# Optimization experiments

Measured on AMD Instinct MI355X. Metric: run time of the kernel, lower is better.

## Reference

```python
import jax, jax.numpy as jnp
import numpy as np

V, D, NH, T_MAX, L, MLP = 50257, 1024, 16, 1024, 12, 4
HD = D // NH
F = D * MLP
B, T = 2, 1024


def setup_inputs() -> dict:
    key = jax.random.key(0)
    ks = jax.random.split(key, 16)
    s = 0.02
    inp = {
        'tokens': jax.random.randint(ks[0], (B, T), 0, V, dtype=jnp.int32),
        'wte': jax.random.normal(ks[1], (V, D), jnp.float32) * s,
        'wpe': jax.random.normal(ks[2], (T_MAX, D), jnp.float32) * s,
        'ln1_w': jnp.ones((L, D)), 'ln1_b': jnp.zeros((L, D)),
        'attn_w': jax.random.normal(ks[3], (L, D, 3 * D), jnp.float32) * s,
        'attn_b': jnp.zeros((L, 3 * D)),
        'aproj_w': jax.random.normal(ks[4], (L, D, D), jnp.float32) * s,
        'aproj_b': jnp.zeros((L, D)),
        'ln2_w': jnp.ones((L, D)), 'ln2_b': jnp.zeros((L, D)),
        'fc_w': jax.random.normal(ks[5], (L, D, F), jnp.float32) * s,
        'fc_b': jnp.zeros((L, F)),
        'proj_w': jax.random.normal(ks[6], (L, F, D), jnp.float32) * s,
        'proj_b': jnp.zeros((L, D)),
        'lnf_w': jnp.ones((D,)), 'lnf_b': jnp.zeros((D,)),
    }
    return inp


def _ln(x, w, b, eps=1e-5):
    m = jnp.mean(x, -1, keepdims=True)
    v = jnp.var(x, -1, keepdims=True)
    return (x - m) * jax.lax.rsqrt(v + eps) * w + b


def _forward(tokens, wte, wpe, ln1_w, ln1_b, attn_w, attn_b, aproj_w, aproj_b,
             ln2_w, ln2_b, fc_w, fc_b, proj_w, proj_b, lnf_w, lnf_b):
    b, t = tokens.shape
    x = wte[tokens] + wpe[:t]  # [B,T,D]
    scale = HD ** -0.5
    causal = jnp.tril(jnp.ones((t, t), bool))  # [T,T]

    def block(x, p):
        l1w, l1b, aw, ab, apw, apb, l2w, l2b, fw, fb, pw, pb = p
        h = _ln(x, l1w, l1b)
        qkv = h @ aw + ab  # [B,T,3D]
        q, k, v = jnp.split(qkv, 3, axis=-1)
        # rearrange 'b t (h n) -> b n t h' with n=NH: last dim is (head_size, n_heads)
        def split_heads(u):
            return u.reshape(b, t, HD, NH).transpose(0, 3, 1, 2)  # [B,NH,T,HD]
        q, k, v = split_heads(q), split_heads(k), split_heads(v)
        scores = jnp.einsum('bnth,bnsh->bnts', q, k) * scale
        scores = jnp.where(causal, scores, -jnp.inf)
        w = jax.nn.softmax(scores, axis=-1)
        att = jnp.einsum('bnts,bnsh->bnth', w, v)
        # rearrange 'b n t h -> b t (n h)'
        att = att.transpose(0, 2, 1, 3).reshape(b, t, D)
        x = x + (att @ apw + apb)
        h2 = _ln(x, l2w, l2b)
        x = x + (jax.nn.gelu(h2 @ fw + fb, approximate=False) @ pw + pb)
        return x, None

    params = (ln1_w, ln1_b, attn_w, attn_b, aproj_w, aproj_b,
              ln2_w, ln2_b, fc_w, fc_b, proj_w, proj_b)
    x, _ = jax.lax.scan(block, x, params)
    x = _ln(x, lnf_w, lnf_b)[:, -1:, :]  # [B,1,D]
    return x @ wte.T  # tied lm_head -> [B,1,V]


def reference(tokens, wte, wpe, ln1_w, ln1_b, attn_w, attn_b, aproj_w, aproj_b,
              ln2_w, ln2_b, fc_w, fc_b, proj_w, proj_b, lnf_w, lnf_b):
    return _forward(tokens, wte, wpe, ln1_w, ln1_b, attn_w, attn_b, aproj_w,
                    aproj_b, ln2_w, ln2_b, fc_w, fc_b, proj_w, proj_b, lnf_w, lnf_b)
```

## Files before the change

kernel.cpp:

```cpp
#include <hip/hip_runtime.h>
#include <cstdint>
#include <math.h>


using u16 = unsigned short;
using bf16x8 = __attribute__((ext_vector_type(8))) short;
using f32x4 = __attribute__((ext_vector_type(4))) float;

#define GLDS16(g, l)                                                        \
  __builtin_amdgcn_global_load_lds(                                         \
      (const __attribute__((address_space(1))) void*)(g),                   \
      (__attribute__((address_space(3))) void*)(l), 16, 0, 0)

__device__ __forceinline__ u16 f2bf(float f) {
  union { float f; unsigned u; } t; t.f = f;
  unsigned r = t.u + 0x7fffu + ((t.u >> 16) & 1u);
  return (u16)(r >> 16);
}
__device__ __forceinline__ float bf2f(u16 v) {
  union { unsigned u; float f; } t; t.u = ((unsigned)v) << 16;
  return t.f;
}

__device__ __forceinline__ float fast_erf(float x) {
  float ax = fabsf(x);
  float t = 1.f / (1.f + 0.3275911f * ax);
  float y = t * (0.254829592f +
            t * (-0.284496736f +
            t * (1.421413741f +
            t * (-1.453152027f +
            t * 1.061405429f))));
  float r = 1.f - y * __expf(-ax * ax);
  return copysignf(r, x);
}

#define DD 1024
#define TTT 1024
#define MR 2048
#define FFF 4096
#define VVV 50257

__global__ __launch_bounds__(256) void k_embed(const int* __restrict__ tokens,
                                               const float* __restrict__ wte,
                                               const float* __restrict__ wpe,
                                               float* __restrict__ x) {
  int m = blockIdx.x, d = threadIdx.x * 4;
  int t = m & (TTT - 1);
  int tok = tokens[m];
  const float4 a = *(const float4*)(wte + (size_t)tok * DD + d);
  const float4 p = *(const float4*)(wpe + (size_t)t * DD + d);
  float4 o; o.x = a.x + p.x; o.y = a.y + p.y; o.z = a.z + p.z; o.w = a.w + p.w;
  *(float4*)(x + (size_t)m * DD + d) = o;
}

__device__ __forceinline__ void addln_body(float* __restrict__ x,
                                           const u16* __restrict__ pp, int npart,
                                           const float* __restrict__ w,
                                           const float* __restrict__ b,
                                           u16* __restrict__ out, int blk) {
  const int wid = threadIdx.x >> 6, lane = threadIdx.x & 63;
  const int m = blk * 4 + wid;
  float* row = x + (size_t)m * DD;
  float4 v[4];
  float s = 0.f, q = 0.f;
#pragma unroll
  for (int j = 0; j < 4; ++j) {
    v[j] = *(const float4*)(row + j * 256 + lane * 4);
#pragma unroll 4
    for (int p = 0; p < npart; ++p) {
      uint64_t pv = *(const uint64_t*)(pp + (size_t)p * MR * DD + (size_t)m * DD + j * 256 + lane * 4);
      v[j].x += bf2f((u16)(pv));
      v[j].y += bf2f((u16)(pv >> 16));
      v[j].z += bf2f((u16)(pv >> 32));
      v[j].w += bf2f((u16)(pv >> 48));
    }
    if (npart) *(float4*)(row + j * 256 + lane * 4) = v[j];
    s += v[j].x + v[j].y + v[j].z + v[j].w;
    q += v[j].x * v[j].x + v[j].y * v[j].y + v[j].z * v[j].z + v[j].w * v[j].w;
  }
#pragma unroll
  for (int off = 1; off < 64; off <<= 1) { s += __shfl_xor(s, off); q += __shfl_xor(q, off); }
  float mean = s * (1.f / DD);
  float var = q * (1.f / DD) - mean * mean;
  float rs = rsqrtf(var + 1e-5f);
#pragma unroll
  for (int j = 0; j < 4; ++j) {
    const float4 wv = *(const float4*)(w + j * 256 + lane * 4);
    const float4 bv = *(const float4*)(b + j * 256 + lane * 4);
    u16 o[4];
    o[0] = f2bf((v[j].x - mean) * rs * wv.x + bv.x);
    o[1] = f2bf((v[j].y - mean) * rs * wv.y + bv.y);
    o[2] = f2bf((v[j].z - mean) * rs * wv.z + bv.z);
    o[3] = f2bf((v[j].w - mean) * rs * wv.w + bv.w);
    *(uint64_t*)(out + (size_t)m * DD + j * 256 + lane * 4) = *(uint64_t*)o;
  }
}

__global__ __launch_bounds__(256) void k_addln(float* __restrict__ x,
                                               const u16* __restrict__ pp, int npart,
                                               const float* __restrict__ w,
                                               const float* __restrict__ b,
                                               u16* __restrict__ out) {
  addln_body(x, pp, npart, w, b, out, blockIdx.x);
}

__device__ __forceinline__ void wtrans_body(const float* __restrict__ atw,
                                            const float* __restrict__ apw,
                                            const float* __restrict__ fcw,
                                            const float* __restrict__ pjw,
                                            u16* __restrict__ wt, int id) {
  __shared__ u16 tb[64][72];
  const float* W; u16* Wt; int K, N, local, kts; bool perm = false;
  if (id < 768)       { W = atw; Wt = wt;           K = 1024; N = 3072; local = id;        kts = 4; perm = true; }
  else if (id < 1024) { W = apw; Wt = wt + 3145728; K = 1024; N = 1024; local = id - 768;  kts = 4; }
  else if (id < 2048) { W = fcw; Wt = wt + 4194304; K = 1024; N = 4096; local = id - 1024; kts = 4; }
  else                { W = pjw; Wt = wt + 8388608; K = 4096; N = 1024; local = id - 2048; kts = 6; }
  const int k0 = (local & ((1 << kts) - 1)) * 64, n0 = (local >> kts) * 64;
  const int tid = threadIdx.x;
  const int rr = tid >> 4, c4 = (tid & 15) * 4;
#pragma unroll
  for (int i = 0; i < 4; ++i) {
    const int r = rr + i * 16;
    const float4 v = *(const float4*)(W + (size_t)(k0 + r) * N + n0 + c4);
    tb[c4 + 0][r] = f2bf(v.x);
    tb[c4 + 1][r] = f2bf(v.y);
    tb[c4 + 2][r] = f2bf(v.z);
    tb[c4 + 3][r] = f2bf(v.w);
  }
  __syncthreads();
  const int n = tid >> 3, k8 = (tid & 7) * 8;
#pragma unroll
  for (int s = 0; s < 2; ++s) {
    u16 o[8];
#pragma unroll
    for (int j = 0; j < 8; ++j) o[j] = tb[n + s * 32][k8 + j];
    int orow = n0 + n + s * 32;
    if (perm) {
      int part = orow >> 10, w = orow & 1023;
      orow = part * 1024 + (w & 15) * 64 + (w >> 4);
    }
    *(bf16x8*)(Wt + (size_t)orow * K + k0 + k8) = *(bf16x8*)o;
  }
}

__global__ __launch_bounds__(256) void k_prep(float* __restrict__ x,
                                              const u16* __restrict__ pp, int npart,
                                              const float* __restrict__ w,
                                              const float* __restrict__ b,
                                              u16* __restrict__ out,
                                              const float* __restrict__ atw,
                                              const float* __restrict__ apw,
                                              const float* __restrict__ fcw,
                                              const float* __restrict__ pjw,
                                              u16* __restrict__ wt,
                                              const float* __restrict__ ab,
                                              float* __restrict__ pbias) {
  if (blockIdx.x < 512) {
    addln_body(x, pp, npart, w, b, out, blockIdx.x);
  } else if (blockIdx.x == 3584) {
    for (int c = threadIdx.x; c < 3072; c += 256) {
      int part = c >> 10, ww = c & 1023;
      pbias[c] = ab[part * 1024 + (ww & 63) * 16 + (ww >> 6)];
    }
  } else {
    wtrans_body(atw, apw, fcw, pjw, wt, blockIdx.x - 512);
  }
}

template <int EPI>
__global__ __launch_bounds__(256) void k_gemm(const u16* __restrict__ A,
                                              const u16* __restrict__ Bt,
                                              const float* __restrict__ bias,
                                              u16* __restrict__ outb,
                                              u16* __restrict__ pp,
                                              u16* __restrict__ vt,
                                              int M, int N, int K, int KC) {
  __shared__ u16 smem[4][128 * 64];
  const int nbx = gridDim.x, nby = gridDim.y;
  const int nwg = nbx * nby * gridDim.z;
  const int orig = blockIdx.x + nbx * (blockIdx.y + nby * blockIdx.z);
  const int qq = nwg >> 3, rr = nwg & 7;
  const int xcd = orig & 7, pos = orig >> 3;
  const int wg = (xcd < rr ? xcd * (qq + 1) : rr * (qq + 1) + (xcd - rr) * qq) + pos;
  const int bx = wg % nbx;
  const int tmpw = wg / nbx;
  const int by = tmpw % nby, bz = tmpw / nby;

  const int tid = threadIdx.x;
  const int lane = tid & 63, wid = tid >> 6;
  const int wr = wid >> 1, wc = wid & 1;
  const int l15 = lane & 15, l4 = lane >> 4;
  const int sx = l15 & 7;
  const int m0 = bx * 128, n0 = by * 128;
  f32x4 acc[4][4] = {};

  const int srow = tid >> 3;
  const int scol = (((tid & 7) ^ (srow & 7)) * 8);
  const int k0beg = bz * KC;
  const int nt = KC >> 6;

  const u16* Ap = A + (size_t)(m0 + srow) * K + scol;
  const u16* Bp = Bt + (size_t)(n0 + srow) * K + scol;

#define STAGE(buf, k0)                                                      \
  {                                                                         \
    _Pragma("unroll")                                                       \
    for (int it = 0; it < 4; ++it) {                                        \
      GLDS16(Ap + (size_t)it * 32 * K + (k0), (char*)smem[buf] + it * 4096 + tid * 16); \
      GLDS16(Bp + (size_t)it * 32 * K + (k0), (char*)smem[2 + (buf)] + it * 4096 + tid * 16); \
    }                                                                       \
  }

  STAGE(0, k0beg);
  for (int t = 0; t < nt; ++t) {
    if (t + 1 < nt) {
      STAGE((t + 1) & 1, k0beg + (t + 1) * 64);
      asm volatile("s_waitcnt vmcnt(8)" ::: "memory");
    } else {
      asm volatile("s_waitcnt vmcnt(0)" ::: "memory");
    }
    __builtin_amdgcn_sched_barrier(0);
    __builtin_amdgcn_s_barrier();
    __builtin_amdgcn_sched_barrier(0);
    const u16* Ab = smem[t & 1];
    const u16* Bb = smem[2 + (t & 1)];
#pragma unroll
    for (int ks = 0; ks < 2; ++ks) {
      const int ch = ((ks * 4 + l4) ^ sx) * 8;
      bf16x8 af[4], bfr[4];
#pragma unroll
      for (int i = 0; i < 4; ++i)
        af[i] = *(const bf16x8*)(Ab + (wr * 64 + i * 16 + l15) * 64 + ch);
#pragma unroll
      for (int j = 0; j < 4; ++j)
        bfr[j] = *(const bf16x8*)(Bb + (wc * 64 + j * 16 + l15) * 64 + ch);
      __builtin_amdgcn_s_setprio(1);
#pragma unroll
      for (int i = 0; i < 4; ++i)
#pragma unroll
        for (int j = 0; j < 4; ++j)
          acc[i][j] = __builtin_amdgcn_mfma_f32_16x16x32_bf16(af[i], bfr[j], acc[i][j], 0, 0, 0);
      __builtin_amdgcn_s_setprio(0);
    }
    __builtin_amdgcn_sched_barrier(0);
    __builtin_amdgcn_s_barrier();
    __builtin_amdgcn_sched_barrier(0);
  }
#undef STAGE
  u16* eb = (u16*)smem;
#pragma unroll
  for (int j = 0; j < 4; ++j) {
    const int col = wc * 64 + j * 16 + l15;
    const float bs = (EPI == 4 && bz != 0) ? 0.f : bias[n0 + col];
#pragma unroll
    for (int i = 0; i < 4; ++i) {
#pragma unroll
      for (int r = 0; r < 4; ++r) {
        const int row = wr * 64 + i * 16 + l4 * 4 + r;
        float v = acc[i][j][r] + bs;
        if (EPI == 2) v = 0.5f * v * (1.f + fast_erf(v * 0.70710678118f));
        eb[row * 132 + col] = f2bf(v);
      }
    }
  }
  __syncthreads();
  if (EPI == 0 && by >= 16) {
    const int b = m0 >> 10, t0 = m0 & 1023;
    const int col = tid >> 1;
    const int tseg = tid & 1;
    const int gc = n0 + col - 2048;
    const int n = gc >> 6, hh = gc & 63;
    u16* vdst = vt + (((size_t)(b * 16 + n)) * 64 + hh) * TTT + t0 + tseg * 64;
    const u16* es = eb + (tseg * 64) * 132 + col;
#pragma unroll
    for (int s = 0; s < 8; ++s) {
      u16 o[8];
#pragma unroll
      for (int k = 0; k < 8; ++k) o[k] = es[(s * 8 + k) * 132];
      *(bf16x8*)(vdst + s * 8) = *(bf16x8*)o;
    }
  } else {
    const int erow = tid >> 1;
    const int ecol0 = (tid & 1) * 64;
    u16* gout = (EPI == 4) ? (pp + (size_t)bz * M * N) : outb;
    u16* gdst = gout + (size_t)(m0 + erow) * N + n0 + ecol0;
    const u16* esrc = eb + erow * 132 + ecol0;
#pragma unroll
    for (int c = 0; c < 8; ++c)
      *(bf16x8*)(gdst + c * 8) = *(const bf16x8*)(esrc + c * 8);
  }
}

__global__ __launch_bounds__(256) void k_attn(const u16* __restrict__ qkv,
                                              const u16* __restrict__ Vt,
                                              u16* __restrict__ attout) {
  __shared__ u16 Ks[128 * 64];
  __shared__ u16 Vs[64 * 128];
  __shared__ u16 Ps[4][16 * 136];

  const int tid = threadIdx.x;
  const int lane = tid & 63, wid = tid >> 6;
  const int l15 = lane & 15, l4 = lane >> 4;
  const int bn = blockIdx.x;
  const int qtr = 15 - (int)blockIdx.y;
  const int q0 = qtr * 64;
  const int b = bn >> 4, nh = bn & 15;
  const char* Kg0 = (const char*)(qkv + (size_t)b * TTT * 3072 + 1024 + nh * 64);
  const char* Vg0 = (const char*)(Vt + (size_t)bn * 64 * TTT);
  const float CEXP = 0.125f * 1.44269504f;

  int KL[4], Kro[4], Kcb[4], VL[4], Voff[4];
#pragma unroll
  for (int it = 0; it < 4; ++it) {
    int L = it * 4096 + tid * 16;
    KL[it] = L;
    int Ls = L ^ (((L >> 7) & 7) << 4);
    Kro[it] = Ls >> 7; Kcb[it] = Ls & 127;
    VL[it] = L;
    int Ls2 = L ^ (((L >> 8) & 7) << 4);
    Voff[it] = (Ls2 >> 8) * 2048 + (Ls2 & 255);
  }

  const int qrow = q0 + wid * 16 + l15;
  const u16* qsrc = qkv + (size_t)(b * TTT + qrow) * 3072 + nh * 64;
  bf16x8 aq[2];
#pragma unroll
  for (int ks = 0; ks < 2; ++ks)
    aq[ks] = *(const bf16x8*)(qsrc + ks * 32 + l4 * 8);

  float m_run[4], l_part[4];
  f32x4 o[4] = {};
#pragma unroll
  for (int r = 0; r < 4; ++r) { m_run[r] = -1e30f; l_part[r] = 0.f; }

  const int ntk = (qtr >> 1) + 1;
  bf16x8 kreg[4], vreg[4];
#pragma unroll
  for (int it = 0; it < 4; ++it) {
    kreg[it] = *(const bf16x8*)(Kg0 + (size_t)Kro[it] * 6144 + Kcb[it]);
    vreg[it] = *(const bf16x8*)(Vg0 + Voff[it]);
  }
  for (int kt = 0; kt < ntk; ++kt) {
#pragma unroll
    for (int it = 0; it < 4; ++it) {
      *(bf16x8*)((char*)Ks + KL[it]) = kreg[it];
      *(bf16x8*)((char*)Vs + VL[it]) = vreg[it];
    }
    __syncthreads();
    if (kt + 1 < ntk) {
#pragma unroll
      for (int it = 0; it < 4; ++it) {
        kreg[it] = *(const bf16x8*)(Kg0 + (size_t)((kt + 1) * 128 + Kro[it]) * 6144 + Kcb[it]);
        vreg[it] = *(const bf16x8*)(Vg0 + (kt + 1) * 256 + Voff[it]);
      }
    }

    f32x4 sf[8];
#pragma unroll
    for (int cf = 0; cf < 8; ++cf) {
      f32x4 z = {};
#pragma unroll
      for (int ks = 0; ks < 2; ++ks) {
        int P = (cf * 16 + l15) * 128 + (ks * 32 + l4 * 8) * 2;
        bf16x8 kb = *(const bf16x8*)((const char*)Ks + (P ^ (((P >> 7) & 7) << 4)));
        z = __builtin_amdgcn_mfma_f32_16x16x32_bf16(aq[ks], kb, z, 0, 0, 0);
      }
      sf[cf] = z;
    }
    if (kt == ntk - 1) {
#pragma unroll
      for (int cf = 0; cf < 8; ++cf)
#pragma unroll
        for (int r = 0; r < 4; ++r) {
          int kg = kt * 128 + cf * 16 + l15;
          int qg = q0 + wid * 16 + l4 * 4 + r;
          if (kg > qg) sf[cf][r] = -1e30f;
        }
    }
    float fac[4];
#pragma unroll
    for (int r = 0; r < 4; ++r) {
      float tm = fmaxf(fmaxf(fmaxf(sf[0][r], sf[1][r]), fmaxf(sf[2][r], sf[3][r])),
                       fmaxf(fmaxf(sf[4][r], sf[5][r]), fmaxf(sf[6][r], sf[7][r])));
#pragma unroll
      for (int off = 1; off < 16; off <<= 1) tm = fmaxf(tm, __shfl_xor(tm, off));
      if (tm > m_run[r] + 64.f) {
        fac[r] = exp2f((m_run[r] - tm) * CEXP);
        m_run[r] = tm;
      } else {
        fac[r] = 1.f;
      }
      float ps = 0.f;
#pragma unroll
      for (int cf = 0; cf < 8; ++cf) {
        float p = exp2f((sf[cf][r] - m_run[r]) * CEXP);
        sf[cf][r] = p;
        ps += p;
      }
      l_part[r] = l_part[r] * fac[r] + ps;
    }
#pragma unroll
    for (int cf = 0; cf < 8; ++cf)
#pragma unroll
      for (int r = 0; r < 4; ++r)
        Ps[wid][(l4 * 4 + r) * 136 + cf * 16 + l15] = f2bf(sf[cf][r]);
#pragma unroll
    for (int hf = 0; hf < 4; ++hf)
#pragma unroll
      for (int r = 0; r < 4; ++r) o[hf][r] *= fac[r];
    bf16x8 pa[4];
#pragma unroll
    for (int ks = 0; ks < 4; ++ks)
      pa[ks] = *(const bf16x8*)&Ps[wid][l15 * 136 + ks * 32 + l4 * 8];
#pragma unroll
    for (int hf = 0; hf < 4; ++hf) {
#pragma unroll
      for (int ks = 0; ks < 4; ++ks) {
        int P = (hf * 16 + l15) * 256 + (ks * 32 + l4 * 8) * 2;
        bf16x8 vb = *(const bf16x8*)((const char*)Vs + (P ^ (((P >> 8) & 7) << 4)));
        o[hf] = __builtin_amdgcn_mfma_f32_16x16x32_bf16(pa[ks], vb, o[hf], 0, 0, 0);
      }
    }
    __syncthreads();
  }
  float lsum[4];
#pragma unroll
  for (int r = 0; r < 4; ++r) {
    float s = l_part[r];
#pragma unroll
    for (int off = 1; off < 16; off <<= 1) s += __shfl_xor(s, off);
    lsum[r] = s;
  }
#pragma unroll
  for (int hf = 0; hf < 4; ++hf)
#pragma unroll
    for (int r = 0; r < 4; ++r) {
      float val = o[hf][r] / lsum[r];
      size_t row = (size_t)b * TTT + q0 + wid * 16 + l4 * 4 + r;
      attout[row * DD + nh * 64 + hf * 16 + l15] = f2bf(val);
    }
}

__global__ __launch_bounds__(256) void k_head(const float* __restrict__ x,
                                              const u16* __restrict__ pp, int npart,
                                              const float* __restrict__ lnf_w,
                                              const float* __restrict__ lnf_b,
                                              const float* __restrict__ wte,
                                              float* __restrict__ out) {
  __shared__ float xs[2 * DD];
  __shared__ float sm[8];
  int tid = threadIdx.x;
  int wid = tid >> 6, lane = tid & 63;
#pragma unroll
  for (int bb = 0; bb < 2; ++bb) {
    int m = bb * TTT + (TTT - 1);
    float4 v = *(const float4*)(x + (size_t)m * DD + tid * 4);
#pragma unroll 4
    for (int p = 0; p < npart; ++p) {
      uint64_t pv = *(const uint64_t*)(pp + (size_t)p * MR * DD + (size_t)m * DD + tid * 4);
      v.x += bf2f((u16)(pv));
      v.y += bf2f((u16)(pv >> 16));
      v.z += bf2f((u16)(pv >> 32));
      v.w += bf2f((u16)(pv >> 48));
    }
    float s = v.x + v.y + v.z + v.w;
    float q = v.x * v.x + v.y * v.y + v.z * v.z + v.w * v.w;
#pragma unroll
    for (int off = 1; off < 64; off <<= 1) { s += __shfl_xor(s, off); q += __shfl_xor(q, off); }
    if ((tid & 63) == 0) { sm[wid] = s; sm[4 + wid] = q; }
    __syncthreads();
    s = sm[0] + sm[1] + sm[2] + sm[3];
    q = sm[4] + sm[5] + sm[6] + sm[7];
    float mean = s * (1.f / DD);
    float var = q * (1.f / DD) - mean * mean;
    float rs = rsqrtf(var + 1e-5f);
    const float4 wv = *(const float4*)(lnf_w + tid * 4);
    const float4 bv = *(const float4*)(lnf_b + tid * 4);
    float4 o;
    o.x = (v.x - mean) * rs * wv.x + bv.x;
    o.y = (v.y - mean) * rs * wv.y + bv.y;
    o.z = (v.z - mean) * rs * wv.z + bv.z;
    o.w = (v.w - mean) * rs * wv.w + bv.w;
    *(float4*)(xs + bb * DD + tid * 4) = o;
    __syncthreads();
  }
  for (int v = blockIdx.x * 4 + wid; v < VVV; v += gridDim.x * 4) {
    const float* wr = wte + (size_t)v * DD;
    float a0 = 0.f, a1 = 0.f;
#pragma unroll
    for (int j = 0; j < 4; ++j) {
      const float4 wv = *(const float4*)(wr + lane * 16 + j * 4);
      const float4 x0 = *(const float4*)(xs + lane * 16 + j * 4);
      const float4 x1 = *(const float4*)(xs + DD + lane * 16 + j * 4);
      a0 += wv.x * x0.x + wv.y * x0.y + wv.z * x0.z + wv.w * x0.w;
      a1 += wv.x * x1.x + wv.y * x1.y + wv.z * x1.z + wv.w * x1.w;
    }
#pragma unroll
    for (int off = 1; off < 64; off <<= 1) { a0 += __shfl_xor(a0, off); a1 += __shfl_xor(a1, off); }
    if (lane == 0) { out[v] = a0; out[VVV + v] = a1; }
  }
}

extern "C" void kernel_launch(void* const* d_in, const int* in_sizes, int n_in,
                              void* d_out, int out_size, void* d_ws, size_t ws_size,
                              hipStream_t stream) {
  const int* tokens    = (const int*)d_in[0];
  const float* wte     = (const float*)d_in[1];
  const float* wpe     = (const float*)d_in[2];
  const float* ln1_w   = (const float*)d_in[3];
  const float* ln1_b   = (const float*)d_in[4];
  const float* attn_w  = (const float*)d_in[5];
  const float* attn_b  = (const float*)d_in[6];
  const float* aproj_w = (const float*)d_in[7];
  const float* aproj_b = (const float*)d_in[8];
  const float* ln2_w   = (const float*)d_in[9];
  const float* ln2_b   = (const float*)d_in[10];
  const float* fc_w    = (const float*)d_in[11];
  const float* fc_b    = (const float*)d_in[12];
  const float* proj_w  = (const float*)d_in[13];
  const float* proj_b  = (const float*)d_in[14];
  const float* lnf_w   = (const float*)d_in[15];
  const float* lnf_b   = (const float*)d_in[16];

  char* ws = (char*)d_ws;
  float* x    = (float*)(ws);
  u16* h      = (u16*)(ws + (8u << 20));
  u16* wt     = (u16*)(ws + (12u << 20));
  u16* qkv    = (u16*)(ws + (36u << 20));
  u16* Vt     = (u16*)(ws + (52u << 20));
  u16* attb   = (u16*)(ws + (56u << 20));
  u16* mlph   = (u16*)(ws + (36u << 20));
  u16* pp     = (u16*)(ws + (60u << 20));
  float* pbias = (float*)(ws + (92u << 20));
  float* out  = (float*)d_out;

  u16* atw = wt;
  u16* apw = wt + 3145728;
  u16* fcw = wt + 4194304;
  u16* pjw = wt + 8388608;

  k_embed<<<MR, 256, 0, stream>>>(tokens, wte, wpe, x);

  for (int l = 0; l < 12; ++l) {
    k_prep<<<3585, 256, 0, stream>>>(x, pp, l == 0 ? 0 : 4,
                                     ln1_w + l * DD, ln1_b + l * DD, h,
                                     attn_w + (size_t)l * DD * 3 * DD,
                                     aproj_w + (size_t)l * DD * DD,
                                     fc_w + (size_t)l * DD * FFF,
                                     proj_w + (size_t)l * FFF * DD, wt,
                                     attn_b + (size_t)l * 3 * DD, pbias);
    k_gemm<0><<<dim3(16, 24, 1), 256, 0, stream>>>(h, atw, pbias, qkv, nullptr, Vt, MR, 3072, 1024, 1024);
    k_attn<<<dim3(32, 16), 256, 0, stream>>>(qkv, Vt, attb);
    k_gemm<4><<<dim3(16, 8, 4), 256, 0, stream>>>(attb, apw, aproj_b + (size_t)l * DD, nullptr, pp, nullptr, MR, 1024, 1024, 256);
    k_addln<<<512, 256, 0, stream>>>(x, pp, 4, ln2_w + l * DD, ln2_b + l * DD, h);
    k_gemm<2><<<dim3(16, 32, 1), 256, 0, stream>>>(h, fcw, fc_b + (size_t)l * FFF, mlph, nullptr, nullptr, MR, 4096, 1024, 1024);
    k_gemm<4><<<dim3(16, 8, 4), 256, 0, stream>>>(mlph, pjw, proj_b + (size_t)l * DD, nullptr, pp, nullptr, MR, 1024, 4096, 1024);
  }
  k_head<<<512, 256, 0, stream>>>(x, pp, 4, lnf_w, lnf_b, wte, out);
}
```

Before: 1.759 ms.

## Fuse embedding into first prep kernel and halve split-K partitions

The standalone embedding kernel is removed; the first layer's prep kernel now computes wte+wpe directly inside the LayerNorm body, which saves one launch and one read of x. The split-K factor for the attention-projection and MLP-projection GEMMs drops from 4 to 2. This halves the bf16 partial buffers written by those GEMMs and read by the add+LayerNorm and head kernels. The cost is fewer blocks in the projection GEMMs (256 instead of 512), which may lower occupancy on the many-CU device.

Result: no change. 1.732 ms (-1.5%).

```diff
diff --git a/kernel.cpp b/kernel.cpp
--- a/kernel.cpp
+++ b/kernel.cpp
@@ -40,43 +40,48 @@
 #define FFF 4096
 #define VVV 50257
 
-__global__ __launch_bounds__(256) void k_embed(const int* __restrict__ tokens,
-                                               const float* __restrict__ wte,
-                                               const float* __restrict__ wpe,
-                                               float* __restrict__ x) {
-  int m = blockIdx.x, d = threadIdx.x * 4;
-  int t = m & (TTT - 1);
-  int tok = tokens[m];
-  const float4 a = *(const float4*)(wte + (size_t)tok * DD + d);
-  const float4 p = *(const float4*)(wpe + (size_t)t * DD + d);
-  float4 o; o.x = a.x + p.x; o.y = a.y + p.y; o.z = a.z + p.z; o.w = a.w + p.w;
-  *(float4*)(x + (size_t)m * DD + d) = o;
-}
-
 __device__ __forceinline__ void addln_body(float* __restrict__ x,
                                            const u16* __restrict__ pp, int npart,
                                            const float* __restrict__ w,
                                            const float* __restrict__ b,
-                                           u16* __restrict__ out, int blk) {
+                                           u16* __restrict__ out, int blk,
+                                           const int* __restrict__ tokens,
+                                           const float* __restrict__ wte,
+                                           const float* __restrict__ wpe,
+                                           int emb) {
   const int wid = threadIdx.x >> 6, lane = threadIdx.x & 63;
   const int m = blk * 4 + wid;
   float* row = x + (size_t)m * DD;
   float4 v[4];
   float s = 0.f, q = 0.f;
-#pragma unroll
-  for (int j = 0; j < 4; ++j) {
-    v[j] = *(const float4*)(row + j * 256 + lane * 4);
-#pragma unroll 4
-    for (int p = 0; p < npart; ++p) {
-      uint64_t pv = *(const uint64_t*)(pp + (size_t)p * MR * DD + (size_t)m * DD + j * 256 + lane * 4);
-      v[j].x += bf2f((u16)(pv));
-      v[j].y += bf2f((u16)(pv >> 16));
-      v[j].z += bf2f((u16)(pv >> 32));
-      v[j].w += bf2f((u16)(pv >> 48));
-    }
-    if (npart) *(float4*)(row + j * 256 + lane * 4) = v[j];
-    s += v[j].x + v[j].y + v[j].z + v[j].w;
-    q += v[j].x * v[j].x + v[j].y * v[j].y + v[j].z * v[j].z + v[j].w * v[j].w;
+  if (emb) {
+    const int tok = tokens[m];
+    const int t = m & (TTT - 1);
+#pragma unroll
+    for (int j = 0; j < 4; ++j) {
+      const float4 a = *(const float4*)(wte + (size_t)tok * DD + j * 256 + lane * 4);
+      const float4 p = *(const float4*)(wpe + (size_t)t * DD + j * 256 + lane * 4);
+      v[j].x = a.x + p.x; v[j].y = a.y + p.y; v[j].z = a.z + p.z; v[j].w = a.w + p.w;
+      *(float4*)(row + j * 256 + lane * 4) = v[j];
+      s += v[j].x + v[j].y + v[j].z + v[j].w;
+      q += v[j].x * v[j].x + v[j].y * v[j].y + v[j].z * v[j].z + v[j].w * v[j].w;
+    }
+  } else {
+#pragma unroll
+    for (int j = 0; j < 4; ++j) {
+      v[j] = *(const float4*)(row + j * 256 + lane * 4);
+#pragma unroll 2
+      for (int p = 0; p < npart; ++p) {
+        uint64_t pv = *(const uint64_t*)(pp + (size_t)p * MR * DD + (size_t)m * DD + j * 256 + lane * 4);
+        v[j].x += bf2f((u16)(pv));
+        v[j].y += bf2f((u16)(pv >> 16));
+        v[j].z += bf2f((u16)(pv >> 32));
+        v[j].w += bf2f((u16)(pv >> 48));
+      }
+      if (npart) *(float4*)(row + j * 256 + lane * 4) = v[j];
+      s += v[j].x + v[j].y + v[j].z + v[j].w;
+      q += v[j].x * v[j].x + v[j].y * v[j].y + v[j].z * v[j].z + v[j].w * v[j].w;
+    }
   }
 #pragma unroll
   for (int off = 1; off < 64; off <<= 1) { s += __shfl_xor(s, off); q += __shfl_xor(q, off); }
@@ -101,7 +106,7 @@
                                                const float* __restrict__ w,
                                                const float* __restrict__ b,
                                                u16* __restrict__ out) {
-  addln_body(x, pp, npart, w, b, out, blockIdx.x);
+  addln_body(x, pp, npart, w, b, out, blockIdx.x, nullptr, nullptr, nullptr, 0);
 }
 
 __device__ __forceinline__ void wtrans_body(const float* __restrict__ atw,
@@ -154,9 +159,13 @@
                                               const float* __restrict__ pjw,
                                               u16* __restrict__ wt,
                                               const float* __restrict__ ab,
-                                              float* __restrict__ pbias) {
+                                              float* __restrict__ pbias,
+                                              const int* __restrict__ tokens,
+                                              const float* __restrict__ wte,
+                                              const float* __restrict__ wpe,
+                                              int emb) {
   if (blockIdx.x < 512) {
-    addln_body(x, pp, npart, w, b, out, blockIdx.x);
+    addln_body(x, pp, npart, w, b, out, blockIdx.x, tokens, wte, wpe, emb);
   } else if (blockIdx.x == 3584) {
     for (int c = threadIdx.x; c < 3072; c += 256) {
       int part = c >> 10, ww = c & 1023;
@@ -455,7 +464,7 @@
   for (int bb = 0; bb < 2; ++bb) {
     int m = bb * TTT + (TTT - 1);
     float4 v = *(const float4*)(x + (size_t)m * DD + tid * 4);
-#pragma unroll 4
+#pragma unroll 2
     for (int p = 0; p < npart; ++p) {
       uint64_t pv = *(const uint64_t*)(pp + (size_t)p * MR * DD + (size_t)m * DD + tid * 4);
       v.x += bf2f((u16)(pv));
@@ -539,22 +548,21 @@
   u16* fcw = wt + 4194304;
   u16* pjw = wt + 8388608;
 
-  k_embed<<<MR, 256, 0, stream>>>(tokens, wte, wpe, x);
-
   for (int l = 0; l < 12; ++l) {
-    k_prep<<<3585, 256, 0, stream>>>(x, pp, l == 0 ? 0 : 4,
+    k_prep<<<3585, 256, 0, stream>>>(x, pp, 2,
                                      ln1_w + l * DD, ln1_b + l * DD, h,
                                      attn_w + (size_t)l * DD * 3 * DD,
                                      aproj_w + (size_t)l * DD * DD,
                                      fc_w + (size_t)l * DD * FFF,
                                      proj_w + (size_t)l * FFF * DD, wt,
-                                     attn_b + (size_t)l * 3 * DD, pbias);
+                                     attn_b + (size_t)l * 3 * DD, pbias,
+                                     tokens, wte, wpe, l == 0 ? 1 : 0);
     k_gemm<0><<<dim3(16, 24, 1), 256, 0, stream>>>(h, atw, pbias, qkv, nullptr, Vt, MR, 3072, 1024, 1024);
     k_attn<<<dim3(32, 16), 256, 0, stream>>>(qkv, Vt, attb);
-    k_gemm<4><<<dim3(16, 8, 4), 256, 0, stream>>>(attb, apw, aproj_b + (size_t)l * DD, nullptr, pp, nullptr, MR, 1024, 1024, 256);
-    k_addln<<<512, 256, 0, stream>>>(x, pp, 4, ln2_w + l * DD, ln2_b + l * DD, h);
+    k_gemm<4><<<dim3(16, 8, 2), 256, 0, stream>>>(attb, apw, aproj_b + (size_t)l * DD, nullptr, pp, nullptr, MR, 1024, 1024, 512);
+    k_addln<<<512, 256, 0, stream>>>(x, pp, 2, ln2_w + l * DD, ln2_b + l * DD, h);
     k_gemm<2><<<dim3(16, 32, 1), 256, 0, stream>>>(h, fcw, fc_b + (size_t)l * FFF, mlph, nullptr, nullptr, MR, 4096, 1024, 1024);
-    k_gemm<4><<<dim3(16, 8, 4), 256, 0, stream>>>(mlph, pjw, proj_b + (size_t)l * DD, nullptr, pp, nullptr, MR, 1024, 4096, 1024);
-  }
-  k_head<<<512, 256, 0, stream>>>(x, pp, 4, lnf_w, lnf_b, wte, out);
-}
+    k_gemm<4><<<dim3(16, 8, 2), 256, 0, stream>>>(mlph, pjw, proj_b + (size_t)l * DD, nullptr, pp, nullptr, MR, 1024, 4096, 2048);
+  }
+  k_head<<<512, 256, 0, stream>>>(x, pp, 2, lnf_w, lnf_b, wte, out);
+}
```
